# Kernel tuning notes

Measured on AMD Instinct MI355X. Metric: run time of the kernel, lower is better.

Reference implementation:

```python
import jax, jax.numpy as jnp
import numpy as np

IN_F, OUT_F = 2048, 2048
IQ, OQ = IN_F // 4, OUT_F // 4
B, S = 4, 4096


def _xavier(key, shape):
    fan_out, fan_in = shape
    limit = float(np.sqrt(6.0 / (fan_in + fan_out)))
    return jax.random.uniform(key, shape, jnp.float32, -limit, limit)


def setup_inputs() -> dict:
    key = jax.random.key(0)
    kx, kr, ki, kj, kk = jax.random.split(key, 5)
    return {
        "x": jax.random.normal(kx, (B, S, IN_F), dtype=jnp.float32),
        "wr": _xavier(kr, (OQ, IQ)),
        "wi": _xavier(ki, (OQ, IQ)),
        "wj": _xavier(kj, (OQ, IQ)),
        "wk": _xavier(kk, (OQ, IQ)),
        "bias": jnp.zeros((OUT_F,), dtype=jnp.float32),
    }


def reference(x, wr, wi, wj, wk, bias):
    b, s, _ = x.shape
    iq = wr.shape[1]
    oq = wr.shape[0]
    # strided quaternion component extraction: x[..., c::4] -> (B*S, iq)
    xq = x.reshape(b * s, iq, 4)  # last-dim interleaved layout
    xr, xi, xj, xk = xq[..., 0], xq[..., 1], xq[..., 2], xq[..., 3]
    # small GEMMs against W^T (W is (oq, iq)); only the products actually used
    Ar = xr @ wr.T
    Br = xi @ wr.T
    Cr = xj @ wr.T
    Dr = xk @ wr.T
    Ai = xr @ wi.T
    Bi = xi @ wi.T
    Aj = xr @ wj.T
    Cj = xj @ wj.T
    Ak = xr @ wk.T
    Dk = xk @ wk.T
    # combine exactly as in the original module
    or_ = Ar - Bi - Cj - Dk
    oi_ = Br + Ai + Dk - Cj
    oj_ = Cr - Dk + Aj + Bi
    ok_ = Dr + Cj - Bi + Ak
    # interleaved scatter: out[:, c::4] = o<c>
    out = jnp.stack([or_, oi_, oj_, ok_], axis=-1).reshape(b, s, 4 * oq)
    return out + bias[None, None, :]
```

## Files before the change

kernel.cpp:

```cpp
#include <hip/hip_runtime.h>


typedef unsigned short u16;
typedef __bf16 bf16x8 __attribute__((ext_vector_type(8)));
typedef float f32x4 __attribute__((ext_vector_type(4)));

#define QM 16384
#define QN 2048
#define QK 2048

__device__ __forceinline__ u16 f2bf(float f) {
    union { float f; unsigned u; } v;
    v.f = f;
    unsigned r = v.u + 0x7FFFu + ((v.u >> 16) & 1u);
    return (u16)(r >> 16);
}

__device__ __forceinline__ void async_copy16(const u16* g, u16* l) {
    __builtin_amdgcn_global_load_lds(
        (const __attribute__((address_space(1))) void*)g,
        (__attribute__((address_space(3))) void*)l,
        16, 0, 0);
}

__global__ void prep_kernel(const float* __restrict__ x, u16* __restrict__ xb,
                            const float* __restrict__ wr, const float* __restrict__ wi,
                            const float* __restrict__ wj, const float* __restrict__ wk,
                            u16* __restrict__ wb) {
    const int b = blockIdx.x;
    if (b < 4096) {
        const int n4 = (QM * QK) / 4;
        for (int i = b * blockDim.x + threadIdx.x; i < n4; i += 4096 * blockDim.x) {
            float4 v = reinterpret_cast<const float4*>(x)[i];
            ushort4 o;
            o.x = f2bf(v.x); o.y = f2bf(v.y); o.z = f2bf(v.z); o.w = f2bf(v.w);
            reinterpret_cast<ushort4*>(xb)[i] = o;
        }
    } else {
        int i = (b - 4096) * blockDim.x + threadIdx.x;
        int n = i >> 9;
        int p = i & 511;
        int q = n >> 2, co = n & 3;
        int base = (q << 9) + p;
        float r  = wr[base], ii = wi[base], jj = wj[base], kk = wk[base];
        float e0, e1, e2, e3;
        if      (co == 0) { e0 = r;  e1 = -ii; e2 = -jj; e3 = -kk; }
        else if (co == 1) { e0 = ii; e1 = r;   e2 = -jj; e3 = kk;  }
        else if (co == 2) { e0 = jj; e1 = ii;  e2 = r;   e3 = -kk; }
        else              { e0 = kk; e1 = -ii; e2 = jj;  e3 = r;   }
        ushort4 o;
        o.x = f2bf(e0); o.y = f2bf(e1); o.z = f2bf(e2); o.w = f2bf(e3);
        reinterpret_cast<ushort4*>(wb)[(n << 9) + p] = o;
    }
}

__global__ __launch_bounds__(512, 2) void qgemm_kernel(const u16* __restrict__ A,
                                                       const u16* __restrict__ B,
                                                       const float* __restrict__ bias,
                                                       float* __restrict__ C) {
    __shared__ __align__(16) u16 L[81920];

    const int bid = blockIdx.x;
    const int swz = (bid & 7) * 64 + (bid >> 3);
    const int bm = swz >> 3;
    const int bn = swz & 7;

    const int tid = threadIdx.x;
    const int wid = tid >> 6, lane = tid & 63;
    const int wm = wid >> 2, wn = wid & 3;
    const int lr = lane & 15, lg = lane >> 4;

    const u16* Asrc = A + (size_t)bm * 256 * QK;
    const u16* Bsrc = B + (size_t)bn * 256 * QK;

    const int rA  = tid >> 3;
    const int clA = ((tid & 7) ^ (rA & 7)) << 3;
    const size_t soff = (size_t)rA * QK + clA;

    f32x4 acc[8][4];
#pragma unroll
    for (int i = 0; i < 8; ++i)
#pragma unroll
        for (int j = 0; j < 4; ++j)
            acc[i][j] = (f32x4){0.f, 0.f, 0.f, 0.f};

    auto stage = [&](const u16* src, int lbase, int k0) {
#pragma unroll
        for (int o = 0; o < 2; ++o)
            async_copy16(src + (size_t)(o * 64) * QK + k0 + soff,
                         &L[lbase + o * 4096 + wid * 512]);
    };

    auto rdA = [&](const u16* LA, int mf, int ks) -> bf16x8 {
        const int r = wm * 128 + mf * 16 + lr;
        const int c = ((ks * 4 + lg) ^ (r & 7)) << 3;
        return *(const bf16x8*)&LA[r * 64 + c];
    };
    auto rdB = [&](const u16* LB, int nf, int ks) -> bf16x8 {
        const int r = wn * 64 + nf * 16 + lr;
        const int c = ((ks * 4 + lg) ^ (r & 7)) << 3;
        return *(const bf16x8*)&LB[r * 64 + c];
    };

    auto doTile = [&](const int ab, const int bt, const int bt2, const int t)
        __attribute__((always_inline)) {
        const u16* LA = &L[ab * 16384];
        const u16* LB = &L[32768 + bt * 16384];
        const int tw1 = (t + 1) & 31, tw2 = (t + 2) & 31;
        const int oA = (ab ^ 1) * 16384;
        const int oB = 32768 + bt2 * 16384;

        bf16x8 a0[4], a1[4], b0[4], b1[4];

#pragma unroll
        for (int nf = 0; nf < 4; ++nf) b0[nf] = rdB(LB, nf, 0);
#pragma unroll
        for (int mf = 0; mf < 4; ++mf) a0[mf] = rdA(LA, mf, 0);
        stage(Asrc, oA, tw1 * 64);
#pragma unroll
        for (int mf = 0; mf < 4; ++mf)
#pragma unroll
            for (int nf = 0; nf < 4; ++nf)
                acc[mf][nf] = __builtin_amdgcn_mfma_f32_16x16x32_bf16(a0[mf], b0[nf], acc[mf][nf], 0, 0, 0);

#pragma unroll
        for (int mf = 0; mf < 4; ++mf) a1[mf] = rdA(LA, 4 + mf, 0);
#pragma unroll
        for (int nf = 0; nf < 4; ++nf) b1[nf] = rdB(LB, nf, 1);
        stage(Asrc + 128 * QK, oA + 8192, tw1 * 64);
#pragma unroll
        for (int mf = 0; mf < 4; ++mf)
#pragma unroll
            for (int nf = 0; nf < 4; ++nf)
                acc[4 + mf][nf] = __builtin_amdgcn_mfma_f32_16x16x32_bf16(a1[mf], b0[nf], acc[4 + mf][nf], 0, 0, 0);

#pragma unroll
        for (int mf = 0; mf < 4; ++mf) a0[mf] = rdA(LA, mf, 1);
        stage(Bsrc, oB, tw2 * 64);
#pragma unroll
        for (int mf = 0; mf < 4; ++mf)
#pragma unroll
            for (int nf = 0; nf < 4; ++nf)
                acc[mf][nf] = __builtin_amdgcn_mfma_f32_16x16x32_bf16(a0[mf], b1[nf], acc[mf][nf], 0, 0, 0);

#pragma unroll
        for (int mf = 0; mf < 4; ++mf) a1[mf] = rdA(LA, 4 + mf, 1);
        stage(Bsrc + 128 * QK, oB + 8192, tw2 * 64);
#pragma unroll
        for (int mf = 0; mf < 4; ++mf)
#pragma unroll
            for (int nf = 0; nf < 4; ++nf)
                acc[4 + mf][nf] = __builtin_amdgcn_mfma_f32_16x16x32_bf16(a1[mf], b1[nf], acc[4 + mf][nf], 0, 0, 0);

        asm volatile("s_waitcnt lgkmcnt(0) vmcnt(4)" ::: "memory");
        __builtin_amdgcn_s_barrier();
    };

    stage(Asrc,            0,             0);
    stage(Asrc + 128 * QK, 8192,          0);
    stage(Bsrc,            32768,             0);
    stage(Bsrc + 128 * QK, 32768 + 8192,      0);
    stage(Bsrc,            32768 + 16384,        64);
    stage(Bsrc + 128 * QK, 32768 + 16384 + 8192, 64);
    asm volatile("s_waitcnt vmcnt(4)" ::: "memory");
    __builtin_amdgcn_s_barrier();

    for (int t = 0; t < 30; t += 6) {
        doTile(0, 0, 2, t);
        doTile(1, 1, 0, t + 1);
        doTile(0, 2, 1, t + 2);
        doTile(1, 0, 2, t + 3);
        doTile(0, 1, 0, t + 4);
        doTile(1, 2, 1, t + 5);
    }
    doTile(0, 0, 2, 30);
    doTile(1, 1, 0, 31);

    const int colbase = bn * 256 + wn * 64;
    const int rowbase = bm * 256 + wm * 128;
    float bsv[4];
#pragma unroll
    for (int nf = 0; nf < 4; ++nf) bsv[nf] = bias[colbase + nf * 16 + lr];
    float* Cb = C + (size_t)rowbase * QN + colbase;
#pragma unroll
    for (int mf = 0; mf < 8; ++mf)
#pragma unroll
        for (int nf = 0; nf < 4; ++nf)
#pragma unroll
            for (int v = 0; v < 4; ++v)
                Cb[(size_t)(mf * 16 + lg * 4 + v) * QN + nf * 16 + lr] = acc[mf][nf][v] + bsv[nf];
}

extern "C" void kernel_launch(void* const* d_in, const int* in_sizes, int n_in,
                              void* d_out, int out_size, void* d_ws, size_t ws_size,
                              hipStream_t stream) {
    const float* x    = (const float*)d_in[0];
    const float* wr   = (const float*)d_in[1];
    const float* wi   = (const float*)d_in[2];
    const float* wj   = (const float*)d_in[3];
    const float* wk   = (const float*)d_in[4];
    const float* bias = (const float*)d_in[5];
    float* out = (float*)d_out;

    u16* xb = (u16*)d_ws;
    u16* wb = (u16*)((char*)d_ws + (size_t)QM * QK * 2);

    prep_kernel<<<8192, 256, 0, stream>>>(x, xb, wr, wi, wj, wk, wb);
    qgemm_kernel<<<512, 512, 0, stream>>>(xb, wb, bias, out);
}
```

Before: 159.1 us.

## Use 1024-thread blocks with smaller per-wave 64x64 tiles in quaternion GEMM

Doubles the block to 16 waves, so each wave owns a 64x64 output sub-tile instead of 128x64. This halves the accumulator registers per thread and adjusts staging so each thread issues one async copy per stage call, with waitcnt thresholds changed to match. The aim is more waves in flight to hide latency. In exchange it adds more LDS reads per MFMA (lower register-level reuse), more barrier participants, and launch_bounds(1024,4) that may not be achievable given the 160KB LDS use.

```diff
diff --git a/kernel.cpp b/kernel.cpp
--- a/kernel.cpp
+++ b/kernel.cpp
@@ -54,10 +54,10 @@
     }
 }
 
-__global__ __launch_bounds__(512, 2) void qgemm_kernel(const u16* __restrict__ A,
-                                                       const u16* __restrict__ B,
-                                                       const float* __restrict__ bias,
-                                                       float* __restrict__ C) {
+__global__ __launch_bounds__(1024, 4) void qgemm_kernel(const u16* __restrict__ A,
+                                                        const u16* __restrict__ B,
+                                                        const float* __restrict__ bias,
+                                                        float* __restrict__ C) {
     __shared__ __align__(16) u16 L[81920];
 
     const int bid = blockIdx.x;
@@ -77,22 +77,19 @@
     const int clA = ((tid & 7) ^ (rA & 7)) << 3;
     const size_t soff = (size_t)rA * QK + clA;
 
-    f32x4 acc[8][4];
+    f32x4 acc[4][4];
 #pragma unroll
-    for (int i = 0; i < 8; ++i)
+    for (int i = 0; i < 4; ++i)
 #pragma unroll
         for (int j = 0; j < 4; ++j)
             acc[i][j] = (f32x4){0.f, 0.f, 0.f, 0.f};
 
     auto stage = [&](const u16* src, int lbase, int k0) {
-#pragma unroll
-        for (int o = 0; o < 2; ++o)
-            async_copy16(src + (size_t)(o * 64) * QK + k0 + soff,
-                         &L[lbase + o * 4096 + wid * 512]);
+        async_copy16(src + k0 + soff, &L[lbase + wid * 512]);
     };
 
     auto rdA = [&](const u16* LA, int mf, int ks) -> bf16x8 {
-        const int r = wm * 128 + mf * 16 + lr;
+        const int r = wm * 64 + mf * 16 + lr;
         const int c = ((ks * 4 + lg) ^ (r & 7)) << 3;
         return *(const bf16x8*)&LA[r * 64 + c];
     };
@@ -110,49 +107,37 @@
         const int oA = (ab ^ 1) * 16384;
         const int oB = 32768 + bt2 * 16384;
 
-        bf16x8 a0[4], a1[4], b0[4], b1[4];
+        {
+            bf16x8 a[4], b[4];
+#pragma unroll
+            for (int nf = 0; nf < 4; ++nf) b[nf] = rdB(LB, nf, 0);
+#pragma unroll
+            for (int mf = 0; mf < 4; ++mf) a[mf] = rdA(LA, mf, 0);
+            stage(Asrc,            oA,        tw1 * 64);
+            stage(Asrc + 128 * QK, oA + 8192, tw1 * 64);
+#pragma unroll
+            for (int mf = 0; mf < 4; ++mf)
+#pragma unroll
+                for (int nf = 0; nf < 4; ++nf)
+                    acc[mf][nf] = __builtin_amdgcn_mfma_f32_16x16x32_bf16(a[mf], b[nf], acc[mf][nf], 0, 0, 0);
+        }
 
+        {
+            bf16x8 a[4], b[4];
 #pragma unroll
-        for (int nf = 0; nf < 4; ++nf) b0[nf] = rdB(LB, nf, 0);
+            for (int nf = 0; nf < 4; ++nf) b[nf] = rdB(LB, nf, 1);
 #pragma unroll
-        for (int mf = 0; mf < 4; ++mf) a0[mf] = rdA(LA, mf, 0);
-        stage(Asrc, oA, tw1 * 64);
+            for (int mf = 0; mf < 4; ++mf) a[mf] = rdA(LA, mf, 1);
+            stage(Bsrc,            oB,        tw2 * 64);
+            stage(Bsrc + 128 * QK, oB + 8192, tw2 * 64);
 #pragma unroll
-        for (int mf = 0; mf < 4; ++mf)
+            for (int mf = 0; mf < 4; ++mf)
 #pragma unroll
-            for (int nf = 0; nf < 4; ++nf)
-                acc[mf][nf] = __builtin_amdgcn_mfma_f32_16x16x32_bf16(a0[mf], b0[nf], acc[mf][nf], 0, 0, 0);
+                for (int nf = 0; nf < 4; ++nf)
+                    acc[mf][nf] = __builtin_amdgcn_mfma_f32_16x16x32_bf16(a[mf], b[nf], acc[mf][nf], 0, 0, 0);
+        }
 
-#pragma unroll
-        for (int mf = 0; mf < 4; ++mf) a1[mf] = rdA(LA, 4 + mf, 0);
-#pragma unroll
-        for (int nf = 0; nf < 4; ++nf) b1[nf] = rdB(LB, nf, 1);
-        stage(Asrc + 128 * QK, oA + 8192, tw1 * 64);
-#pragma unroll
-        for (int mf = 0; mf < 4; ++mf)
-#pragma unroll
-            for (int nf = 0; nf < 4; ++nf)
-                acc[4 + mf][nf] = __builtin_amdgcn_mfma_f32_16x16x32_bf16(a1[mf], b0[nf], acc[4 + mf][nf], 0, 0, 0);
-
-#pragma unroll
-        for (int mf = 0; mf < 4; ++mf) a0[mf] = rdA(LA, mf, 1);
-        stage(Bsrc, oB, tw2 * 64);
-#pragma unroll
-        for (int mf = 0; mf < 4; ++mf)
-#pragma unroll
-            for (int nf = 0; nf < 4; ++nf)
-                acc[mf][nf] = __builtin_amdgcn_mfma_f32_16x16x32_bf16(a0[mf], b1[nf], acc[mf][nf], 0, 0, 0);
-
-#pragma unroll
-        for (int mf = 0; mf < 4; ++mf) a1[mf] = rdA(LA, 4 + mf, 1);
-        stage(Bsrc + 128 * QK, oB + 8192, tw2 * 64);
-#pragma unroll
-        for (int mf = 0; mf < 4; ++mf)
-#pragma unroll
-            for (int nf = 0; nf < 4; ++nf)
-                acc[4 + mf][nf] = __builtin_amdgcn_mfma_f32_16x16x32_bf16(a1[mf], b1[nf], acc[4 + mf][nf], 0, 0, 0);
-
-        asm volatile("s_waitcnt lgkmcnt(0) vmcnt(4)" ::: "memory");
+        asm volatile("s_waitcnt lgkmcnt(0) vmcnt(2)" ::: "memory");
         __builtin_amdgcn_s_barrier();
     };
 
@@ -162,7 +147,7 @@
     stage(Bsrc + 128 * QK, 32768 + 8192,      0);
     stage(Bsrc,            32768 + 16384,        64);
     stage(Bsrc + 128 * QK, 32768 + 16384 + 8192, 64);
-    asm volatile("s_waitcnt vmcnt(4)" ::: "memory");
+    asm volatile("s_waitcnt vmcnt(2)" ::: "memory");
     __builtin_amdgcn_s_barrier();
 
     for (int t = 0; t < 30; t += 6) {
@@ -177,13 +162,13 @@
     doTile(1, 1, 0, 31);
 
     const int colbase = bn * 256 + wn * 64;
-    const int rowbase = bm * 256 + wm * 128;
+    const int rowbase = bm * 256 + wm * 64;
     float bsv[4];
 #pragma unroll
     for (int nf = 0; nf < 4; ++nf) bsv[nf] = bias[colbase + nf * 16 + lr];
     float* Cb = C + (size_t)rowbase * QN + colbase;
 #pragma unroll
-    for (int mf = 0; mf < 8; ++mf)
+    for (int mf = 0; mf < 4; ++mf)
 #pragma unroll
         for (int nf = 0; nf < 4; ++nf)
 #pragma unroll
@@ -206,5 +191,5 @@
     u16* wb = (u16*)((char*)d_ws + (size_t)QM * QK * 2);
 
     prep_kernel<<<8192, 256, 0, stream>>>(x, xb, wr, wi, wj, wk, wb);
-    qgemm_kernel<<<512, 512, 0, stream>>>(xb, wb, bias, out);
+    qgemm_kernel<<<512, 1024, 0, stream>>>(xb, wb, bias, out);
 }
```

After: 172.3 us. 8.3% more time.

## Fuse fp32-to-bf16 conversion of activations into GEMM A-tile loading

Applied to the files above, without the earlier changes.

Drops the separate pass that converted the whole fp32 input to bf16 in a workspace. The GEMM now loads fp32 A tiles into registers, converts them to bf16 and writes them to LDS at the end of each tile step, while B still uses async global-to-LDS copies. This removes a full read and write of the converted activation tensor plus its re-read. In exchange, A traffic into the GEMM doubles (fp32), more registers are live across the MFMA sequence, and the vmcnt wait accounting now mixes register loads with async copies.

```diff
diff --git a/kernel.cpp b/kernel.cpp
--- a/kernel.cpp
+++ b/kernel.cpp
@@ -3,6 +3,7 @@
 
 typedef unsigned short u16;
 typedef __bf16 bf16x8 __attribute__((ext_vector_type(8)));
+typedef unsigned short u16x8 __attribute__((ext_vector_type(8)));
 typedef float f32x4 __attribute__((ext_vector_type(4)));
 
 #define QM 16384
@@ -23,38 +24,27 @@
         16, 0, 0);
 }
 
-__global__ void prep_kernel(const float* __restrict__ x, u16* __restrict__ xb,
-                            const float* __restrict__ wr, const float* __restrict__ wi,
-                            const float* __restrict__ wj, const float* __restrict__ wk,
-                            u16* __restrict__ wb) {
-    const int b = blockIdx.x;
-    if (b < 4096) {
-        const int n4 = (QM * QK) / 4;
-        for (int i = b * blockDim.x + threadIdx.x; i < n4; i += 4096 * blockDim.x) {
-            float4 v = reinterpret_cast<const float4*>(x)[i];
-            ushort4 o;
-            o.x = f2bf(v.x); o.y = f2bf(v.y); o.z = f2bf(v.z); o.w = f2bf(v.w);
-            reinterpret_cast<ushort4*>(xb)[i] = o;
-        }
-    } else {
-        int i = (b - 4096) * blockDim.x + threadIdx.x;
-        int n = i >> 9;
-        int p = i & 511;
-        int q = n >> 2, co = n & 3;
-        int base = (q << 9) + p;
-        float r  = wr[base], ii = wi[base], jj = wj[base], kk = wk[base];
-        float e0, e1, e2, e3;
-        if      (co == 0) { e0 = r;  e1 = -ii; e2 = -jj; e3 = -kk; }
-        else if (co == 1) { e0 = ii; e1 = r;   e2 = -jj; e3 = kk;  }
-        else if (co == 2) { e0 = jj; e1 = ii;  e2 = r;   e3 = -kk; }
-        else              { e0 = kk; e1 = -ii; e2 = jj;  e3 = r;   }
-        ushort4 o;
-        o.x = f2bf(e0); o.y = f2bf(e1); o.z = f2bf(e2); o.w = f2bf(e3);
-        reinterpret_cast<ushort4*>(wb)[(n << 9) + p] = o;
-    }
-}
-
-__global__ __launch_bounds__(512, 2) void qgemm_kernel(const u16* __restrict__ A,
+__global__ void prepw_kernel(const float* __restrict__ wr, const float* __restrict__ wi,
+                             const float* __restrict__ wj, const float* __restrict__ wk,
+                             u16* __restrict__ wb) {
+    int i = blockIdx.x * blockDim.x + threadIdx.x;
+    if (i >= QN * (QK / 4)) return;
+    int n = i >> 9;
+    int p = i & 511;
+    int q = n >> 2, co = n & 3;
+    int base = (q << 9) + p;
+    float r  = wr[base], ii = wi[base], jj = wj[base], kk = wk[base];
+    float e0, e1, e2, e3;
+    if      (co == 0) { e0 = r;  e1 = -ii; e2 = -jj; e3 = -kk; }
+    else if (co == 1) { e0 = ii; e1 = r;   e2 = -jj; e3 = kk;  }
+    else if (co == 2) { e0 = jj; e1 = ii;  e2 = r;   e3 = -kk; }
+    else              { e0 = kk; e1 = -ii; e2 = jj;  e3 = r;   }
+    ushort4 o;
+    o.x = f2bf(e0); o.y = f2bf(e1); o.z = f2bf(e2); o.w = f2bf(e3);
+    reinterpret_cast<ushort4*>(wb)[(n << 9) + p] = o;
+}
+
+__global__ __launch_bounds__(512, 2) void qgemm_kernel(const float* __restrict__ X,
                                                        const u16* __restrict__ B,
                                                        const float* __restrict__ bias,
                                                        float* __restrict__ C) {
@@ -70,12 +60,13 @@
     const int wm = wid >> 2, wn = wid & 3;
     const int lr = lane & 15, lg = lane >> 4;
 
-    const u16* Asrc = A + (size_t)bm * 256 * QK;
-    const u16* Bsrc = B + (size_t)bn * 256 * QK;
-
-    const int rA  = tid >> 3;
-    const int clA = ((tid & 7) ^ (rA & 7)) << 3;
-    const size_t soff = (size_t)rA * QK + clA;
+    const float* Afp = X + (size_t)bm * 256 * QK;
+    const u16*  Bsrc = B + (size_t)bn * 256 * QK;
+
+    const int rA   = tid >> 3;
+    const int aclf = ((tid & 7) ^ (rA & 7)) << 3;
+    const size_t bsoff = (size_t)rA * QK + aclf;
+    const int ldst = wid * 512 + lane * 8;
 
     f32x4 acc[8][4];
 #pragma unroll
@@ -84,11 +75,31 @@
         for (int j = 0; j < 4; ++j)
             acc[i][j] = (f32x4){0.f, 0.f, 0.f, 0.f};
 
-    auto stage = [&](const u16* src, int lbase, int k0) {
+    auto stageB = [&](const u16* src, int lbase, int k0) {
 #pragma unroll
         for (int o = 0; o < 2; ++o)
-            async_copy16(src + (size_t)(o * 64) * QK + k0 + soff,
+            async_copy16(src + (size_t)(o * 64) * QK + k0 + bsoff,
                          &L[lbase + o * 4096 + wid * 512]);
+    };
+
+    auto loadA = [&](f32x4 (&af)[4][2], int k0) {
+#pragma unroll
+        for (int c = 0; c < 4; ++c) {
+            const float* s = Afp + (size_t)(rA + (c & 1) * 64 + (c >> 1) * 128) * QK + aclf + k0;
+            af[c][0] = *(const f32x4*)(s);
+            af[c][1] = *(const f32x4*)(s + 4);
+        }
+    };
+    auto writeA = [&](f32x4 (&af)[4][2], int lbase) {
+#pragma unroll
+        for (int c = 0; c < 4; ++c) {
+            u16x8 p;
+#pragma unroll
+            for (int e = 0; e < 4; ++e) p[e]     = f2bf(af[c][0][e]);
+#pragma unroll
+            for (int e = 0; e < 4; ++e) p[4 + e] = f2bf(af[c][1][e]);
+            *reinterpret_cast<u16x8*>(&L[lbase + (c >> 1) * 8192 + (c & 1) * 4096 + ldst]) = p;
+        }
     };
 
     auto rdA = [&](const u16* LA, int mf, int ks) -> bf16x8 {
@@ -111,12 +122,13 @@
         const int oB = 32768 + bt2 * 16384;
 
         bf16x8 a0[4], a1[4], b0[4], b1[4];
+        f32x4 af[4][2];
 
 #pragma unroll
         for (int nf = 0; nf < 4; ++nf) b0[nf] = rdB(LB, nf, 0);
 #pragma unroll
         for (int mf = 0; mf < 4; ++mf) a0[mf] = rdA(LA, mf, 0);
-        stage(Asrc, oA, tw1 * 64);
+        loadA(af, tw1 * 64);
 #pragma unroll
         for (int mf = 0; mf < 4; ++mf)
 #pragma unroll
@@ -127,7 +139,6 @@
         for (int mf = 0; mf < 4; ++mf) a1[mf] = rdA(LA, 4 + mf, 0);
 #pragma unroll
         for (int nf = 0; nf < 4; ++nf) b1[nf] = rdB(LB, nf, 1);
-        stage(Asrc + 128 * QK, oA + 8192, tw1 * 64);
 #pragma unroll
         for (int mf = 0; mf < 4; ++mf)
 #pragma unroll
@@ -136,7 +147,7 @@
 
 #pragma unroll
         for (int mf = 0; mf < 4; ++mf) a0[mf] = rdA(LA, mf, 1);
-        stage(Bsrc, oB, tw2 * 64);
+        stageB(Bsrc, oB, tw2 * 64);
 #pragma unroll
         for (int mf = 0; mf < 4; ++mf)
 #pragma unroll
@@ -145,25 +156,30 @@
 
 #pragma unroll
         for (int mf = 0; mf < 4; ++mf) a1[mf] = rdA(LA, 4 + mf, 1);
-        stage(Bsrc + 128 * QK, oB + 8192, tw2 * 64);
+        stageB(Bsrc + 128 * QK, oB + 8192, tw2 * 64);
 #pragma unroll
         for (int mf = 0; mf < 4; ++mf)
 #pragma unroll
             for (int nf = 0; nf < 4; ++nf)
                 acc[4 + mf][nf] = __builtin_amdgcn_mfma_f32_16x16x32_bf16(a1[mf], b1[nf], acc[4 + mf][nf], 0, 0, 0);
+
+        writeA(af, oA);
 
         asm volatile("s_waitcnt lgkmcnt(0) vmcnt(4)" ::: "memory");
         __builtin_amdgcn_s_barrier();
     };
 
-    stage(Asrc,            0,             0);
-    stage(Asrc + 128 * QK, 8192,          0);
-    stage(Bsrc,            32768,             0);
-    stage(Bsrc + 128 * QK, 32768 + 8192,      0);
-    stage(Bsrc,            32768 + 16384,        64);
-    stage(Bsrc + 128 * QK, 32768 + 16384 + 8192, 64);
-    asm volatile("s_waitcnt vmcnt(4)" ::: "memory");
-    __builtin_amdgcn_s_barrier();
+    {
+        f32x4 af[4][2];
+        loadA(af, 0);
+        stageB(Bsrc,            32768,             0);
+        stageB(Bsrc + 128 * QK, 32768 + 8192,      0);
+        stageB(Bsrc,            32768 + 16384,        64);
+        stageB(Bsrc + 128 * QK, 32768 + 16384 + 8192, 64);
+        writeA(af, 0);
+        asm volatile("s_waitcnt lgkmcnt(0) vmcnt(4)" ::: "memory");
+        __builtin_amdgcn_s_barrier();
+    }
 
     for (int t = 0; t < 30; t += 6) {
         doTile(0, 0, 2, t);
@@ -202,9 +218,8 @@
     const float* bias = (const float*)d_in[5];
     float* out = (float*)d_out;
 
-    u16* xb = (u16*)d_ws;
-    u16* wb = (u16*)((char*)d_ws + (size_t)QM * QK * 2);
-
-    prep_kernel<<<8192, 256, 0, stream>>>(x, xb, wr, wi, wj, wk, wb);
-    qgemm_kernel<<<512, 512, 0, stream>>>(xb, wb, bias, out);
-}
+    u16* wb = (u16*)d_ws;
+
+    prepw_kernel<<<4096, 256, 0, stream>>>(wr, wi, wj, wk, wb);
+    qgemm_kernel<<<512, 512, 0, stream>>>(x, wb, bias, out);
+}
```

Measured after the change: 218.4 us. 1.37x slower.

## Triple-buffer A tiles and prefetch next tile's first fragments across barrier

Applied to the files above, without the earlier changes.

Swaps the LDS buffering, giving A three stages and B two. The first A/B fragments of the next K-tile are now read into registers before the tile ends, so each tile's first MFMA block starts without waiting on LDS reads. A mid-tile barrier with a looser vmcnt lets the B stage land while MFMAs continue. This adds register pressure from the carried fragments and a second barrier per tile, and makes the buffer-rotation indexing more intricate.

```diff
diff --git a/kernel.cpp b/kernel.cpp
--- a/kernel.cpp
+++ b/kernel.cpp
@@ -102,79 +102,90 @@
         return *(const bf16x8*)&LB[r * 64 + c];
     };
 
-    auto doTile = [&](const int ab, const int bt, const int bt2, const int t)
-        __attribute__((always_inline)) {
-        const u16* LA = &L[ab * 16384];
-        const u16* LB = &L[32768 + bt * 16384];
+    bf16x8 aC[4], bC[4];
+
+    auto doTile = [&](const int cA, const int nA, const int sA, const int cB,
+                      const int t) __attribute__((always_inline)) {
+        const u16* LA  = &L[cA * 16384];
+        const u16* LB  = &L[49152 + cB * 16384];
+        const u16* LAn = &L[nA * 16384];
+        const u16* LBn = &L[49152 + (cB ^ 1) * 16384];
+        const int oB = 49152 + (cB ^ 1) * 16384;
+        const int oA = sA * 16384;
         const int tw1 = (t + 1) & 31, tw2 = (t + 2) & 31;
-        const int oA = (ab ^ 1) * 16384;
-        const int oB = 32768 + bt2 * 16384;
-
-        bf16x8 a0[4], a1[4], b0[4], b1[4];
-
-#pragma unroll
-        for (int nf = 0; nf < 4; ++nf) b0[nf] = rdB(LB, nf, 0);
-#pragma unroll
-        for (int mf = 0; mf < 4; ++mf) a0[mf] = rdA(LA, mf, 0);
-        stage(Asrc, oA, tw1 * 64);
-#pragma unroll
-        for (int mf = 0; mf < 4; ++mf)
-#pragma unroll
-            for (int nf = 0; nf < 4; ++nf)
-                acc[mf][nf] = __builtin_amdgcn_mfma_f32_16x16x32_bf16(a0[mf], b0[nf], acc[mf][nf], 0, 0, 0);
-
-#pragma unroll
-        for (int mf = 0; mf < 4; ++mf) a1[mf] = rdA(LA, 4 + mf, 0);
-#pragma unroll
-        for (int nf = 0; nf < 4; ++nf) b1[nf] = rdB(LB, nf, 1);
-        stage(Asrc + 128 * QK, oA + 8192, tw1 * 64);
-#pragma unroll
-        for (int mf = 0; mf < 4; ++mf)
-#pragma unroll
-            for (int nf = 0; nf < 4; ++nf)
-                acc[4 + mf][nf] = __builtin_amdgcn_mfma_f32_16x16x32_bf16(a1[mf], b0[nf], acc[4 + mf][nf], 0, 0, 0);
-
-#pragma unroll
-        for (int mf = 0; mf < 4; ++mf) a0[mf] = rdA(LA, mf, 1);
-        stage(Bsrc, oB, tw2 * 64);
-#pragma unroll
-        for (int mf = 0; mf < 4; ++mf)
-#pragma unroll
-            for (int nf = 0; nf < 4; ++nf)
-                acc[mf][nf] = __builtin_amdgcn_mfma_f32_16x16x32_bf16(a0[mf], b1[nf], acc[mf][nf], 0, 0, 0);
-
-#pragma unroll
-        for (int mf = 0; mf < 4; ++mf) a1[mf] = rdA(LA, 4 + mf, 1);
-        stage(Bsrc + 128 * QK, oB + 8192, tw2 * 64);
-#pragma unroll
-        for (int mf = 0; mf < 4; ++mf)
-#pragma unroll
-            for (int nf = 0; nf < 4; ++nf)
-                acc[4 + mf][nf] = __builtin_amdgcn_mfma_f32_16x16x32_bf16(a1[mf], b1[nf], acc[4 + mf][nf], 0, 0, 0);
-
-        asm volatile("s_waitcnt lgkmcnt(0) vmcnt(4)" ::: "memory");
+
+        bf16x8 aN[4], aM[4], bN[4], aP[4];
+
+#pragma unroll
+        for (int mf = 0; mf < 4; ++mf) aN[mf] = rdA(LA, 4 + mf, 0);
+        stage(Bsrc, oB, tw1 * 64);
+#pragma unroll
+        for (int mf = 0; mf < 4; ++mf)
+#pragma unroll
+            for (int nf = 0; nf < 4; ++nf)
+                acc[mf][nf] = __builtin_amdgcn_mfma_f32_16x16x32_bf16(aC[mf], bC[nf], acc[mf][nf], 0, 0, 0);
+
+#pragma unroll
+        for (int mf = 0; mf < 4; ++mf) aM[mf] = rdA(LA, mf, 1);
+#pragma unroll
+        for (int nf = 0; nf < 4; ++nf) bN[nf] = rdB(LB, nf, 1);
+        stage(Bsrc + 128 * QK, oB + 8192, tw1 * 64);
+#pragma unroll
+        for (int mf = 0; mf < 4; ++mf)
+#pragma unroll
+            for (int nf = 0; nf < 4; ++nf)
+                acc[4 + mf][nf] = __builtin_amdgcn_mfma_f32_16x16x32_bf16(aN[mf], bC[nf], acc[4 + mf][nf], 0, 0, 0);
+
+#pragma unroll
+        for (int mf = 0; mf < 4; ++mf) aP[mf] = rdA(LA, 4 + mf, 1);
+        stage(Asrc, oA, tw2 * 64);
+#pragma unroll
+        for (int mf = 0; mf < 4; ++mf)
+#pragma unroll
+            for (int nf = 0; nf < 4; ++nf)
+                acc[mf][nf] = __builtin_amdgcn_mfma_f32_16x16x32_bf16(aM[mf], bN[nf], acc[mf][nf], 0, 0, 0);
+
+        asm volatile("s_waitcnt vmcnt(2)" ::: "memory");
+        __builtin_amdgcn_s_barrier();
+
+#pragma unroll
+        for (int mf = 0; mf < 4; ++mf) aC[mf] = rdA(LAn, mf, 0);
+#pragma unroll
+        for (int nf = 0; nf < 4; ++nf) bC[nf] = rdB(LBn, nf, 0);
+        stage(Asrc + 128 * QK, oA + 8192, tw2 * 64);
+#pragma unroll
+        for (int mf = 0; mf < 4; ++mf)
+#pragma unroll
+            for (int nf = 0; nf < 4; ++nf)
+                acc[4 + mf][nf] = __builtin_amdgcn_mfma_f32_16x16x32_bf16(aP[mf], bN[nf], acc[4 + mf][nf], 0, 0, 0);
+
+        asm volatile("s_waitcnt vmcnt(4)" ::: "memory");
         __builtin_amdgcn_s_barrier();
     };
 
     stage(Asrc,            0,             0);
     stage(Asrc + 128 * QK, 8192,          0);
-    stage(Bsrc,            32768,             0);
-    stage(Bsrc + 128 * QK, 32768 + 8192,      0);
-    stage(Bsrc,            32768 + 16384,        64);
-    stage(Bsrc + 128 * QK, 32768 + 16384 + 8192, 64);
+    stage(Bsrc,            49152,             0);
+    stage(Bsrc + 128 * QK, 49152 + 8192,      0);
+    stage(Asrc,            16384,            64);
+    stage(Asrc + 128 * QK, 16384 + 8192,     64);
     asm volatile("s_waitcnt vmcnt(4)" ::: "memory");
     __builtin_amdgcn_s_barrier();
+#pragma unroll
+    for (int mf = 0; mf < 4; ++mf) aC[mf] = rdA(&L[0], mf, 0);
+#pragma unroll
+    for (int nf = 0; nf < 4; ++nf) bC[nf] = rdB(&L[49152], nf, 0);
 
     for (int t = 0; t < 30; t += 6) {
-        doTile(0, 0, 2, t);
-        doTile(1, 1, 0, t + 1);
-        doTile(0, 2, 1, t + 2);
-        doTile(1, 0, 2, t + 3);
-        doTile(0, 1, 0, t + 4);
-        doTile(1, 2, 1, t + 5);
+        doTile(0, 1, 2, 0, t);
+        doTile(1, 2, 0, 1, t + 1);
+        doTile(2, 0, 1, 0, t + 2);
+        doTile(0, 1, 2, 1, t + 3);
+        doTile(1, 2, 0, 0, t + 4);
+        doTile(2, 0, 1, 1, t + 5);
     }
-    doTile(0, 0, 2, 30);
-    doTile(1, 1, 0, 31);
+    doTile(0, 1, 2, 0, 30);
+    doTile(1, 2, 0, 1, 31);
 
     const int colbase = bn * 256 + wn * 64;
     const int rowbase = bm * 256 + wm * 128;
```

Result: slower. 177.2 us (+11.4%).
